# Performance work log

Measured on AMD Instinct MI355X. Metric: run time of the kernel, lower is better.

The kernel has to match this reference:

```python
import jax, jax.numpy as jnp
import numpy as np

B, LQ, LK, DQ, DKEY, DV = 8, 2048, 2048, 1024, 1024, 1024
MASK_NEG = -1e6  # d2l masked_softmax fill value


def setup_inputs() -> dict:
    key = jax.random.key(0)
    kq, kk, kv, kl, kw = jax.random.split(key, 5)
    queries = jax.random.normal(kq, (B, LQ, DQ), dtype=jnp.float32)
    keys = jax.random.normal(kk, (B, LK, DKEY), dtype=jnp.float32)
    values = jax.random.normal(kv, (B, LK, DV), dtype=jnp.float32)
    valid_lens = jax.random.randint(kl, (B,), 1, LK + 1)
    W_q = jax.random.normal(kw, (DQ, DKEY), dtype=jnp.float32) / np.sqrt(DQ)
    return {"queries": queries, "keys": keys, "values": values,
            "valid_lens": valid_lens, "W_q": W_q}


def reference(queries, keys, values, valid_lens, W_q):
    # Q projection: LazyLinear(key_dim, bias=False)
    q = jnp.einsum("bqd,dk->bqk", queries, W_q)          # [B, LQ, DKEY]
    d = q.shape[-1]
    scores = jnp.einsum("bqk,bsk->bqs", q, keys) / jnp.sqrt(jnp.asarray(d, q.dtype))
    # masked_softmax: positions >= valid_len set to -1e6 before softmax
    mask = jnp.arange(scores.shape[-1])[None, None, :] < valid_lens[:, None, None]
    scores = jnp.where(mask, scores, MASK_NEG)
    attn = jax.nn.softmax(scores, axis=-1)               # [B, LQ, LK]
    # dropout p=0.0 (eval) -> identity
    return jnp.einsum("bqs,bsv->bqv", attn, values)      # [B, LQ, DV]
```

## Files before the change

### kernel.cpp

```cpp
#include <hip/hip_runtime.h>
#include <cstdint>
#include <cstddef>

#define B_   8
#define LQ_  2048
#define LK_  2048

typedef __attribute__((ext_vector_type(8))) __bf16 bf16x8;
typedef __attribute__((ext_vector_type(4))) float f32x4;
typedef __attribute__((ext_vector_type(8))) unsigned short ushortx8;

__device__ __forceinline__ unsigned short f2bf(float f) {
  unsigned u = __builtin_bit_cast(unsigned, f);
  u = u + 0x7fffu + ((u >> 16) & 1u);
  return (unsigned short)(u >> 16);
}
__device__ __forceinline__ float bf2f(unsigned short h) {
  unsigned u = ((unsigned)h) << 16;
  return __builtin_bit_cast(float, u);
}

__device__ __forceinline__ void gld_lds16(const void* g, void* l) {
  __builtin_amdgcn_global_load_lds((__attribute__((address_space(1))) void*)(void*)g,
                                   (__attribute__((address_space(3))) void*)l, 16, 0, 0);
}

__global__ __launch_bounds__(256) void cast3_bf16_kernel(
    const float* __restrict__ q, unsigned short* __restrict__ qo,
    const float* __restrict__ k, unsigned short* __restrict__ ko,
    const float* __restrict__ w, unsigned short* __restrict__ wo,
    const int* __restrict__ vlp) {
  int bb = (int)blockIdx.x;
  const float* in;
  unsigned short* out;
  if (bb < 8192) {
    in = q; out = qo;
  } else if (bb < 16384) {
    bb -= 8192;
    in = k; out = ko;
    int batch = bb >> 10;
    int row = (bb & 1023) * 2;
    int vl = vlp[batch];
    if (row >= ((vl + 255) & ~255)) return;
  } else {
    bb -= 16384;
    in = w; out = wo;
  }
  size_t i = ((size_t)bb * 256 + threadIdx.x) * 8;
  float4 a = *(const float4*)(in + i);
  float4 b = *(const float4*)(in + i + 4);
  ushortx8 o;
  o[0] = f2bf(a.x); o[1] = f2bf(a.y); o[2] = f2bf(a.z); o[3] = f2bf(a.w);
  o[4] = f2bf(b.x); o[5] = f2bf(b.y); o[6] = f2bf(b.z); o[7] = f2bf(b.w);
  *(ushortx8*)(out + i) = o;
}

__global__ __launch_bounds__(256) void transpose_cast_kernel(
    const float* __restrict__ in, unsigned short* __restrict__ out,
    int R, int C, long in_bstride, long out_bstride, const int* __restrict__ vlp) {
  __shared__ float t[32][33];
  int r0 = blockIdx.y * 32;
  if (vlp) {
    int kEnd = (vlp[blockIdx.z] + 63) & ~63;
    if (r0 >= kEnd) return;
  }
  const float* inb = in + (size_t)blockIdx.z * in_bstride;
  unsigned short* outb = out + (size_t)blockIdx.z * out_bstride;
  int c0 = blockIdx.x * 32;
  int tx = threadIdx.x, ty = threadIdx.y;
#pragma unroll
  for (int k = 0; k < 4; ++k) {
    int r = ty + k * 8;
    t[r][tx] = inb[(size_t)(r0 + r) * C + c0 + tx];
  }
  __syncthreads();
#pragma unroll
  for (int k = 0; k < 4; ++k) {
    int c = ty + k * 8;
    outb[(size_t)(c0 + c) * R + r0 + tx] = f2bf(t[tx][c]);
  }
}

template <int OUTM, int SKIPN, int SKIPM, int CLAMPK>
__global__ __launch_bounds__(512, 2) void gemm256_kernel(
    const unsigned short* __restrict__ A, const unsigned short* __restrict__ B,
    void* __restrict__ Cp, int M, int N, int K,
    long a_bstride, long b_bstride, long c_bstride, float scale,
    const int* __restrict__ vlp) {
  __shared__ unsigned short lds[4][2][128 * 64];

  const int tid = threadIdx.x;
  const int wid = tid >> 6;
  const int lane = tid & 63;
  const int lane15 = lane & 15;
  const int lhalf = lane >> 4;

  const int nt = (int)((blockIdx.x + 2 * blockIdx.z) & (gridDim.x - 1));
  const int m0 = blockIdx.y * 256;
  const int n0 = nt * 256;

  int vl = K;
  if constexpr (SKIPN || SKIPM || CLAMPK) vl = vlp[blockIdx.z];
  if constexpr (SKIPN) {
    if (n0 >= vl) return;
  }
  if constexpr (SKIPM) {
    if (m0 >= vl) return;
  }
  int kEnd = K;
  if constexpr (CLAMPK) {
    int ke = (vl + 63) & ~63;
    kEnd = ke < K ? ke : K;
  }
  const int nKt = kEnd >> 5;

  const unsigned short* Ab = A + (size_t)blockIdx.z * a_bstride;
  const unsigned short* Bb = B + (size_t)blockIdx.z * b_bstride;

  int srowA[2], srowB[2], scol[2], sdst[2];
#pragma unroll
  for (int j = 0; j < 2; ++j) {
    int blk = (wid * 2 + j) * 64 + lane;
    int p = blk >> 3, q = blk & 7;
    int c = q ^ (p & 7);
    int r = 2 * p + (c >> 2);
    scol[j] = (c & 3) * 8;
    srowA[j] = m0 + r;
    srowB[j] = n0 + r;
    sdst[j] = blk * 8;
  }

  const int om = (wid >> 2) * 128;
  const int on = (wid & 3) * 64;
  const int swz8 = ((((lane15 & 1) << 2) + lhalf) ^ ((lane15 >> 1) & 7)) << 3;
  const int aBase = ((om >> 1) + (lane15 >> 1)) * 64 + swz8;
  const int bBase = ((on >> 1) + (lane15 >> 1)) * 64 + swz8;

  f32x4 acc[8][4];
#pragma unroll
  for (int f = 0; f < 8; ++f)
#pragma unroll
    for (int g = 0; g < 4; ++g) acc[f][g] = (f32x4){0.f, 0.f, 0.f, 0.f};

#pragma unroll
  for (int j = 0; j < 2; ++j)
    gld_lds16(Ab + (size_t)srowA[j] * K + scol[j], &lds[0][0][sdst[j]]);
#pragma unroll
  for (int j = 0; j < 2; ++j)
    gld_lds16(Bb + (size_t)srowB[j] * K + scol[j], &lds[0][1][sdst[j]]);
#pragma unroll
  for (int j = 0; j < 2; ++j)
    gld_lds16(Ab + (size_t)srowA[j] * K + (32 + scol[j]), &lds[1][0][sdst[j]]);
#pragma unroll
  for (int j = 0; j < 2; ++j)
    gld_lds16(Bb + (size_t)srowB[j] * K + (32 + scol[j]), &lds[1][1][sdst[j]]);
  if (nKt > 2) {
#pragma unroll
    for (int j = 0; j < 2; ++j)
      gld_lds16(Ab + (size_t)srowA[j] * K + (64 + scol[j]), &lds[2][0][sdst[j]]);
#pragma unroll
    for (int j = 0; j < 2; ++j)
      gld_lds16(Bb + (size_t)srowB[j] * K + (64 + scol[j]), &lds[2][1][sdst[j]]);
    asm volatile("s_waitcnt vmcnt(8)" ::: "memory");
  } else {
    asm volatile("s_waitcnt vmcnt(4)" ::: "memory");
  }
  __builtin_amdgcn_s_barrier();

  for (int t = 0; t < nKt; ++t) {
    const unsigned short* lA = &lds[t & 3][0][0];
    const unsigned short* lB = &lds[t & 3][1][0];
    const bool st = (t + 3) < nKt;
    const int nb = (t + 3) & 3;
    const int kc = (t + 3) * 32;

    bf16x8 a0[4], b0[4];
#pragma unroll
    for (int f = 0; f < 4; ++f) a0[f] = *(const bf16x8*)&lA[aBase + f * 512];
#pragma unroll
    for (int g = 0; g < 4; ++g) b0[g] = *(const bf16x8*)&lB[bBase + g * 512];
    if (st) {
#pragma unroll
      for (int j = 0; j < 2; ++j)
        gld_lds16(Ab + (size_t)srowA[j] * K + (kc + scol[j]), &lds[nb][0][sdst[j]]);
    }
    __builtin_amdgcn_s_barrier();
    asm volatile("s_waitcnt lgkmcnt(0)" ::: "memory");
    __builtin_amdgcn_sched_barrier(0);
    __builtin_amdgcn_s_setprio(1);
#pragma unroll
    for (int f = 0; f < 4; ++f)
#pragma unroll
      for (int g = 0; g < 4; ++g)
        acc[f][g] = __builtin_amdgcn_mfma_f32_16x16x32_bf16(a0[f], b0[g], acc[f][g], 0, 0, 0);
    __builtin_amdgcn_s_setprio(0);
    __builtin_amdgcn_s_barrier();

    bf16x8 a1[4];
#pragma unroll
    for (int f = 0; f < 4; ++f) a1[f] = *(const bf16x8*)&lA[aBase + (f + 4) * 512];
    if (st) {
#pragma unroll
      for (int j = 0; j < 2; ++j)
        gld_lds16(Bb + (size_t)srowB[j] * K + (kc + scol[j]), &lds[nb][1][sdst[j]]);
    }
    __builtin_amdgcn_s_barrier();
    asm volatile("s_waitcnt lgkmcnt(0)" ::: "memory");
    __builtin_amdgcn_sched_barrier(0);
    __builtin_amdgcn_s_setprio(1);
#pragma unroll
    for (int f = 0; f < 4; ++f)
#pragma unroll
      for (int g = 0; g < 4; ++g)
        acc[f + 4][g] = __builtin_amdgcn_mfma_f32_16x16x32_bf16(a1[f], b0[g], acc[f + 4][g], 0, 0, 0);
    __builtin_amdgcn_s_setprio(0);
    {
      int hi = nKt < t + 4 ? nKt : t + 4;
      int pend = hi - (t + 2);
      if (pend >= 2)
        asm volatile("s_waitcnt vmcnt(8)" ::: "memory");
      else if (pend == 1)
        asm volatile("s_waitcnt vmcnt(4)" ::: "memory");
      else
        asm volatile("s_waitcnt vmcnt(0)" ::: "memory");
    }
    __builtin_amdgcn_s_barrier();
  }

  const size_t boffC = (size_t)blockIdx.z * c_bstride;
#pragma unroll
  for (int f = 0; f < 8; ++f) {
    int row = m0 + om + f * 16 + lhalf * 4;
#pragma unroll
    for (int g = 0; g < 4; ++g) {
      int col = n0 + on + g * 16 + lane15;
#pragma unroll
      for (int r = 0; r < 4; ++r) {
        float v = acc[f][g][r];
        if constexpr (OUTM == 0) {
          ((unsigned short*)Cp + boffC)[(size_t)(row + r) * N + col] = f2bf(v);
        } else if constexpr (OUTM == 1) {
          ((unsigned short*)Cp + boffC)[(size_t)(row + r) * N + col] = f2bf(v * scale);
        } else {
          ((float*)Cp + boffC)[(size_t)(row + r) * N + col] = v;
        }
      }
    }
  }
}

__global__ __launch_bounds__(256) void softmax_kernel(unsigned short* __restrict__ scores,
                                                      const int* __restrict__ valid_lens) {
  const int row = blockIdx.x;
  const int b = row >> 11;
  const int vl = valid_lens[b];
  const int kEnd = (vl + 63) & ~63;
  unsigned short* rp = scores + (size_t)row * LK_;
  const int tid = threadIdx.x;
  const int wid = tid >> 6, lane = tid & 63;
  __shared__ float sred[4];

  const int cb = tid * 8;
  const bool act = cb < kEnd;
  ushortx8 h = {};
  if (act) h = *(const ushortx8*)(rp + cb);
  float x[8];
#pragma unroll
  for (int t = 0; t < 8; ++t) x[t] = bf2f(h[t]);

  float m = -3.4e38f;
#pragma unroll
  for (int t = 0; t < 8; ++t)
    if (cb + t < vl) m = fmaxf(m, x[t]);
#pragma unroll
  for (int off = 32; off >= 1; off >>= 1) m = fmaxf(m, __shfl_xor(m, off));
  if (lane == 0) sred[wid] = m;
  __syncthreads();
  m = fmaxf(fmaxf(sred[0], sred[1]), fmaxf(sred[2], sred[3]));
  __syncthreads();

  float e[8];
  float s = 0.f;
#pragma unroll
  for (int t = 0; t < 8; ++t) {
    e[t] = (cb + t < vl) ? __expf(x[t] - m) : 0.f;
    s += e[t];
  }
#pragma unroll
  for (int off = 32; off >= 1; off >>= 1) s += __shfl_xor(s, off);
  if (lane == 0) sred[wid] = s;
  __syncthreads();
  s = sred[0] + sred[1] + sred[2] + sred[3];
  float inv = 1.f / s;

  if (act) {
    ushortx8 o;
#pragma unroll
    for (int t = 0; t < 8; ++t) o[t] = f2bf(e[t] * inv);
    *(ushortx8*)(rp + cb) = o;
  }
}

extern "C" void kernel_launch(void* const* d_in, const int* in_sizes, int n_in,
                              void* d_out, int out_size, void* d_ws, size_t ws_size,
                              hipStream_t stream) {
  const float* queries = (const float*)d_in[0];
  const float* keys = (const float*)d_in[1];
  const float* values = (const float*)d_in[2];
  const int* valid_lens = (const int*)d_in[3];
  const float* W_q = (const float*)d_in[4];
  float* out = (float*)d_out;

  unsigned short* ws = (unsigned short*)d_ws;
  const size_t M1 = (size_t)1024 * 1024;
  unsigned short* q_bf = ws;
  unsigned short* scores = ws + 16 * M1;
  unsigned short* keysP = ws + 48 * M1;
  unsigned short* valsT = keysP;
  unsigned short* w_bf = ws + 64 * M1;
  unsigned short* keys_bf = ws + 65 * M1;

  cast3_bf16_kernel<<<dim3(16896), 256, 0, stream>>>(
      queries, q_bf, keys, keys_bf, W_q, w_bf, valid_lens);
  gemm256_kernel<0, 0, 1, 0><<<dim3(4, 8, 8), 512, 0, stream>>>(
      keys_bf, w_bf, keysP, 2048, 1024, 1024,
      (long)2048 * 1024, 0, (long)2048 * 1024, 1.f, valid_lens);
  gemm256_kernel<1, 1, 0, 0><<<dim3(8, 8, 8), 512, 0, stream>>>(
      q_bf, keysP, scores, 2048, 2048, 1024,
      (long)2048 * 1024, (long)2048 * 1024, (long)2048 * 2048, 0.03125f, valid_lens);
  transpose_cast_kernel<<<dim3(32, 64, 8), dim3(32, 8), 0, stream>>>(
      values, valsT, 2048, 1024, (long)2048 * 1024, (long)1024 * 2048, valid_lens);
  softmax_kernel<<<dim3(B_ * LQ_), 256, 0, stream>>>(scores, valid_lens);
  gemm256_kernel<2, 0, 0, 1><<<dim3(4, 8, 8), 512, 0, stream>>>(
      scores, valsT, out, 2048, 1024, 2048,
      (long)2048 * 2048, (long)1024 * 2048, (long)2048 * 1024, 1.f, valid_lens);
}
```

Before: 381.3 us.

## Double-buffer MFMA fragments in registers and cut barriers per K-step

Rewrites the GEMM main loop as a macro, unrolled by two, that ping-pongs two sets of A/B fragment registers. The next K-tile's fragments are read from LDS while the current tile's second MFMA half runs, instead of waiting at the top of each step. Barriers drop from three to one per K-step, and the vmcnt waits are tightened so only the next tile has to have landed. This is meant to hide LDS read latency and synchronisation stalls, at the cost of more registers and an implicit assumption that the K-tile count is even.

```diff
diff --git a/kernel.cpp b/kernel.cpp
--- a/kernel.cpp
+++ b/kernel.cpp
@@ -81,6 +81,70 @@
   }
 }
 
+#define KT_ITER(T, CA0, CB0, NA0, NB0)                                          \
+  {                                                                             \
+    const unsigned short* lA = &lds[(T) & 3][0][0];                             \
+    const unsigned short* lAn = &lds[((T) + 1) & 3][0][0];                      \
+    const unsigned short* lBn = &lds[((T) + 1) & 3][1][0];                      \
+    const bool st = (T) + 3 < nKt;                                              \
+    const int nb = ((T) + 3) & 3;                                               \
+    const int kc = ((T) + 3) * 32;                                              \
+    const bool rd = (T) + 1 < nKt;                                              \
+    bf16x8 a1[4];                                                               \
+    _Pragma("unroll")                                                           \
+    for (int f = 0; f < 4; ++f)                                                 \
+      a1[f] = *(const bf16x8*)&lA[aBase + (f + 4) * 512];                       \
+    if (st) {                                                                   \
+      _Pragma("unroll")                                                         \
+      for (int j = 0; j < 2; ++j)                                               \
+        gld_lds16(Ab + (size_t)srowA[j] * K + (kc + scol[j]),                   \
+                  &lds[nb][0][sdst[j]]);                                        \
+    }                                                                           \
+    __builtin_amdgcn_sched_barrier(0);                                          \
+    __builtin_amdgcn_s_setprio(1);                                              \
+    _Pragma("unroll")                                                           \
+    for (int f = 0; f < 4; ++f) {                                               \
+      _Pragma("unroll")                                                         \
+      for (int g = 0; g < 4; ++g)                                               \
+        acc[f][g] = __builtin_amdgcn_mfma_f32_16x16x32_bf16(CA0[f], CB0[g],     \
+                                                            acc[f][g], 0, 0, 0);\
+    }                                                                           \
+    __builtin_amdgcn_s_setprio(0);                                              \
+    asm volatile("s_waitcnt lgkmcnt(0)" ::: "memory");                          \
+    __builtin_amdgcn_sched_barrier(0);                                          \
+    if (rd) {                                                                   \
+      _Pragma("unroll")                                                         \
+      for (int f = 0; f < 4; ++f)                                               \
+        NA0[f] = *(const bf16x8*)&lAn[aBase + f * 512];                         \
+      _Pragma("unroll")                                                         \
+      for (int g = 0; g < 4; ++g)                                               \
+        NB0[g] = *(const bf16x8*)&lBn[bBase + g * 512];                         \
+    }                                                                           \
+    if (st) {                                                                   \
+      _Pragma("unroll")                                                         \
+      for (int j = 0; j < 2; ++j)                                               \
+        gld_lds16(Bb + (size_t)srowB[j] * K + (kc + scol[j]),                   \
+                  &lds[nb][1][sdst[j]]);                                        \
+    }                                                                           \
+    __builtin_amdgcn_sched_barrier(0);                                          \
+    __builtin_amdgcn_s_setprio(1);                                              \
+    _Pragma("unroll")                                                           \
+    for (int f = 0; f < 4; ++f) {                                               \
+      _Pragma("unroll")                                                         \
+      for (int g = 0; g < 4; ++g)                                               \
+        acc[f + 4][g] = __builtin_amdgcn_mfma_f32_16x16x32_bf16(                \
+            a1[f], CB0[g], acc[f + 4][g], 0, 0, 0);                             \
+    }                                                                           \
+    __builtin_amdgcn_s_setprio(0);                                              \
+    asm volatile("s_waitcnt lgkmcnt(0)" ::: "memory");                          \
+    if (st)                                                                     \
+      asm volatile("s_waitcnt vmcnt(4)" ::: "memory");                          \
+    else                                                                        \
+      asm volatile("s_waitcnt vmcnt(0)" ::: "memory");                          \
+    __builtin_amdgcn_sched_barrier(0);                                          \
+    __builtin_amdgcn_s_barrier();                                               \
+  }
+
 template <int OUTM, int SKIPN, int SKIPM, int CLAMPK>
 __global__ __launch_bounds__(512, 2) void gemm256_kernel(
     const unsigned short* __restrict__ A, const unsigned short* __restrict__ B,
@@ -161,70 +225,23 @@
 #pragma unroll
     for (int j = 0; j < 2; ++j)
       gld_lds16(Bb + (size_t)srowB[j] * K + (64 + scol[j]), &lds[2][1][sdst[j]]);
-    asm volatile("s_waitcnt vmcnt(8)" ::: "memory");
+    asm volatile("s_waitcnt vmcnt(4)" ::: "memory");
   } else {
-    asm volatile("s_waitcnt vmcnt(4)" ::: "memory");
+    asm volatile("s_waitcnt vmcnt(0)" ::: "memory");
   }
   __builtin_amdgcn_s_barrier();
 
-  for (int t = 0; t < nKt; ++t) {
-    const unsigned short* lA = &lds[t & 3][0][0];
-    const unsigned short* lB = &lds[t & 3][1][0];
-    const bool st = (t + 3) < nKt;
-    const int nb = (t + 3) & 3;
-    const int kc = (t + 3) * 32;
-
-    bf16x8 a0[4], b0[4];
-#pragma unroll
-    for (int f = 0; f < 4; ++f) a0[f] = *(const bf16x8*)&lA[aBase + f * 512];
-#pragma unroll
-    for (int g = 0; g < 4; ++g) b0[g] = *(const bf16x8*)&lB[bBase + g * 512];
-    if (st) {
-#pragma unroll
-      for (int j = 0; j < 2; ++j)
-        gld_lds16(Ab + (size_t)srowA[j] * K + (kc + scol[j]), &lds[nb][0][sdst[j]]);
-    }
-    __builtin_amdgcn_s_barrier();
-    asm volatile("s_waitcnt lgkmcnt(0)" ::: "memory");
-    __builtin_amdgcn_sched_barrier(0);
-    __builtin_amdgcn_s_setprio(1);
-#pragma unroll
-    for (int f = 0; f < 4; ++f)
-#pragma unroll
-      for (int g = 0; g < 4; ++g)
-        acc[f][g] = __builtin_amdgcn_mfma_f32_16x16x32_bf16(a0[f], b0[g], acc[f][g], 0, 0, 0);
-    __builtin_amdgcn_s_setprio(0);
-    __builtin_amdgcn_s_barrier();
-
-    bf16x8 a1[4];
-#pragma unroll
-    for (int f = 0; f < 4; ++f) a1[f] = *(const bf16x8*)&lA[aBase + (f + 4) * 512];
-    if (st) {
-#pragma unroll
-      for (int j = 0; j < 2; ++j)
-        gld_lds16(Bb + (size_t)srowB[j] * K + (kc + scol[j]), &lds[nb][1][sdst[j]]);
-    }
-    __builtin_amdgcn_s_barrier();
-    asm volatile("s_waitcnt lgkmcnt(0)" ::: "memory");
-    __builtin_amdgcn_sched_barrier(0);
-    __builtin_amdgcn_s_setprio(1);
-#pragma unroll
-    for (int f = 0; f < 4; ++f)
-#pragma unroll
-      for (int g = 0; g < 4; ++g)
-        acc[f + 4][g] = __builtin_amdgcn_mfma_f32_16x16x32_bf16(a1[f], b0[g], acc[f + 4][g], 0, 0, 0);
-    __builtin_amdgcn_s_setprio(0);
-    {
-      int hi = nKt < t + 4 ? nKt : t + 4;
-      int pend = hi - (t + 2);
-      if (pend >= 2)
-        asm volatile("s_waitcnt vmcnt(8)" ::: "memory");
-      else if (pend == 1)
-        asm volatile("s_waitcnt vmcnt(4)" ::: "memory");
-      else
-        asm volatile("s_waitcnt vmcnt(0)" ::: "memory");
-    }
-    __builtin_amdgcn_s_barrier();
+  bf16x8 a0X[4], b0X[4], a0Y[4], b0Y[4];
+#pragma unroll
+  for (int f = 0; f < 4; ++f) a0X[f] = *(const bf16x8*)&lds[0][0][aBase + f * 512];
+#pragma unroll
+  for (int g = 0; g < 4; ++g) b0X[g] = *(const bf16x8*)&lds[0][1][bBase + g * 512];
+  asm volatile("s_waitcnt lgkmcnt(0)" ::: "memory");
+  __builtin_amdgcn_sched_barrier(0);
+
+  for (int t = 0; t < nKt; t += 2) {
+    KT_ITER(t, a0X, b0X, a0Y, b0Y);
+    KT_ITER(t + 1, a0Y, b0Y, a0X, b0X);
   }
 
   const size_t boffC = (size_t)blockIdx.z * c_bstride;
```

Result: faster. 361.5 us (-5.2%).

## Shrink GEMM tiles to 128x128 with 4 waves and batch-interleaved 1D grid

Applied to the files above, without the earlier changes.

Replaces the 256x256 tile GEMM with 512 threads by a 128x128 tile GEMM with 256 threads and a flattened 1D grid where the batch index is the fastest-varying component. Finer tiles let the valid_len skipping (SKIPN/SKIPM) prune work at 128 granularity, and the key cast now also truncates at 128 rows. The intent is less wasted compute on masked regions and better load balance across CUs. The cost is lower arithmetic intensity per tile and more global/LDS traffic per FLOP. The in-loop pipeline is also simplified to a single MFMA phase per k-step, with one barrier removed.

```diff
diff --git a/kernel.cpp b/kernel.cpp
--- a/kernel.cpp
+++ b/kernel.cpp
@@ -41,7 +41,7 @@
     int batch = bb >> 10;
     int row = (bb & 1023) * 2;
     int vl = vlp[batch];
-    if (row >= ((vl + 255) & ~255)) return;
+    if (row >= ((vl + 127) & ~127)) return;
   } else {
     bb -= 16384;
     in = w; out = wo;
@@ -82,12 +82,12 @@
 }
 
 template <int OUTM, int SKIPN, int SKIPM, int CLAMPK>
-__global__ __launch_bounds__(512, 2) void gemm256_kernel(
+__global__ __launch_bounds__(256, 2) void gemm128_kernel(
     const unsigned short* __restrict__ A, const unsigned short* __restrict__ B,
     void* __restrict__ Cp, int M, int N, int K,
     long a_bstride, long b_bstride, long c_bstride, float scale,
-    const int* __restrict__ vlp) {
-  __shared__ unsigned short lds[4][2][128 * 64];
+    const int* __restrict__ vlp, int lognx) {
+  __shared__ unsigned short lds[4][2][64 * 64];
 
   const int tid = threadIdx.x;
   const int wid = tid >> 6;
@@ -95,12 +95,18 @@
   const int lane15 = lane & 15;
   const int lhalf = lane >> 4;
 
-  const int nt = (int)((blockIdx.x + 2 * blockIdx.z) & (gridDim.x - 1));
-  const int m0 = blockIdx.y * 256;
-  const int n0 = nt * 256;
+  const int idx = (int)blockIdx.x;
+  const int z = idx & 7;
+  const int rest = idx >> 3;
+  const int nxm = (1 << lognx) - 1;
+  const int xt = rest & nxm;
+  const int yt = rest >> lognx;
+  const int nt = (xt + 2 * z) & nxm;
+  const int m0 = yt * 128;
+  const int n0 = nt * 128;
 
   int vl = K;
-  if constexpr (SKIPN || SKIPM || CLAMPK) vl = vlp[blockIdx.z];
+  if constexpr (SKIPN || SKIPM || CLAMPK) vl = vlp[z];
   if constexpr (SKIPN) {
     if (n0 >= vl) return;
   }
@@ -114,8 +120,8 @@
   }
   const int nKt = kEnd >> 5;
 
-  const unsigned short* Ab = A + (size_t)blockIdx.z * a_bstride;
-  const unsigned short* Bb = B + (size_t)blockIdx.z * b_bstride;
+  const unsigned short* Ab = A + (size_t)z * a_bstride;
+  const unsigned short* Bb = B + (size_t)z * b_bstride;
 
   int srowA[2], srowB[2], scol[2], sdst[2];
 #pragma unroll
@@ -130,15 +136,15 @@
     sdst[j] = blk * 8;
   }
 
-  const int om = (wid >> 2) * 128;
-  const int on = (wid & 3) * 64;
+  const int om = (wid & 1) * 64;
+  const int on = (wid >> 1) * 64;
   const int swz8 = ((((lane15 & 1) << 2) + lhalf) ^ ((lane15 >> 1) & 7)) << 3;
   const int aBase = ((om >> 1) + (lane15 >> 1)) * 64 + swz8;
   const int bBase = ((on >> 1) + (lane15 >> 1)) * 64 + swz8;
 
-  f32x4 acc[8][4];
-#pragma unroll
-  for (int f = 0; f < 8; ++f)
+  f32x4 acc[4][4];
+#pragma unroll
+  for (int f = 0; f < 4; ++f)
 #pragma unroll
     for (int g = 0; g < 4; ++g) acc[f][g] = (f32x4){0.f, 0.f, 0.f, 0.f};
 
@@ -174,17 +180,19 @@
     const int nb = (t + 3) & 3;
     const int kc = (t + 3) * 32;
 
-    bf16x8 a0[4], b0[4];
-#pragma unroll
-    for (int f = 0; f < 4; ++f) a0[f] = *(const bf16x8*)&lA[aBase + f * 512];
-#pragma unroll
-    for (int g = 0; g < 4; ++g) b0[g] = *(const bf16x8*)&lB[bBase + g * 512];
+    bf16x8 a[4], b[4];
+#pragma unroll
+    for (int f = 0; f < 4; ++f) a[f] = *(const bf16x8*)&lA[aBase + f * 512];
+#pragma unroll
+    for (int g = 0; g < 4; ++g) b[g] = *(const bf16x8*)&lB[bBase + g * 512];
     if (st) {
 #pragma unroll
       for (int j = 0; j < 2; ++j)
         gld_lds16(Ab + (size_t)srowA[j] * K + (kc + scol[j]), &lds[nb][0][sdst[j]]);
+#pragma unroll
+      for (int j = 0; j < 2; ++j)
+        gld_lds16(Bb + (size_t)srowB[j] * K + (kc + scol[j]), &lds[nb][1][sdst[j]]);
     }
-    __builtin_amdgcn_s_barrier();
     asm volatile("s_waitcnt lgkmcnt(0)" ::: "memory");
     __builtin_amdgcn_sched_barrier(0);
     __builtin_amdgcn_s_setprio(1);
@@ -192,27 +200,7 @@
     for (int f = 0; f < 4; ++f)
 #pragma unroll
       for (int g = 0; g < 4; ++g)
-        acc[f][g] = __builtin_amdgcn_mfma_f32_16x16x32_bf16(a0[f], b0[g], acc[f][g], 0, 0, 0);
-    __builtin_amdgcn_s_setprio(0);
-    __builtin_amdgcn_s_barrier();
-
-    bf16x8 a1[4];
-#pragma unroll
-    for (int f = 0; f < 4; ++f) a1[f] = *(const bf16x8*)&lA[aBase + (f + 4) * 512];
-    if (st) {
-#pragma unroll
-      for (int j = 0; j < 2; ++j)
-        gld_lds16(Bb + (size_t)srowB[j] * K + (kc + scol[j]), &lds[nb][1][sdst[j]]);
-    }
-    __builtin_amdgcn_s_barrier();
-    asm volatile("s_waitcnt lgkmcnt(0)" ::: "memory");
-    __builtin_amdgcn_sched_barrier(0);
-    __builtin_amdgcn_s_setprio(1);
-#pragma unroll
-    for (int f = 0; f < 4; ++f)
-#pragma unroll
-      for (int g = 0; g < 4; ++g)
-        acc[f + 4][g] = __builtin_amdgcn_mfma_f32_16x16x32_bf16(a1[f], b0[g], acc[f + 4][g], 0, 0, 0);
+        acc[f][g] = __builtin_amdgcn_mfma_f32_16x16x32_bf16(a[f], b[g], acc[f][g], 0, 0, 0);
     __builtin_amdgcn_s_setprio(0);
     {
       int hi = nKt < t + 4 ? nKt : t + 4;
@@ -227,9 +215,9 @@
     __builtin_amdgcn_s_barrier();
   }
 
-  const size_t boffC = (size_t)blockIdx.z * c_bstride;
-#pragma unroll
-  for (int f = 0; f < 8; ++f) {
+  const size_t boffC = (size_t)z * c_bstride;
+#pragma unroll
+  for (int f = 0; f < 4; ++f) {
     int row = m0 + om + f * 16 + lhalf * 4;
 #pragma unroll
     for (int g = 0; g < 4; ++g) {
@@ -322,16 +310,16 @@
 
   cast3_bf16_kernel<<<dim3(16896), 256, 0, stream>>>(
       queries, q_bf, keys, keys_bf, W_q, w_bf, valid_lens);
-  gemm256_kernel<0, 0, 1, 0><<<dim3(4, 8, 8), 512, 0, stream>>>(
+  gemm128_kernel<0, 0, 1, 0><<<dim3(16 * 8 * 8), 256, 0, stream>>>(
       keys_bf, w_bf, keysP, 2048, 1024, 1024,
-      (long)2048 * 1024, 0, (long)2048 * 1024, 1.f, valid_lens);
-  gemm256_kernel<1, 1, 0, 0><<<dim3(8, 8, 8), 512, 0, stream>>>(
+      (long)2048 * 1024, 0, (long)2048 * 1024, 1.f, valid_lens, 3);
+  gemm128_kernel<1, 1, 0, 0><<<dim3(16 * 16 * 8), 256, 0, stream>>>(
       q_bf, keysP, scores, 2048, 2048, 1024,
-      (long)2048 * 1024, (long)2048 * 1024, (long)2048 * 2048, 0.03125f, valid_lens);
+      (long)2048 * 1024, (long)2048 * 1024, (long)2048 * 2048, 0.03125f, valid_lens, 4);
   transpose_cast_kernel<<<dim3(32, 64, 8), dim3(32, 8), 0, stream>>>(
       values, valsT, 2048, 1024, (long)2048 * 1024, (long)1024 * 2048, valid_lens);
   softmax_kernel<<<dim3(B_ * LQ_), 256, 0, stream>>>(scores, valid_lens);
-  gemm256_kernel<2, 0, 0, 1><<<dim3(4, 8, 8), 512, 0, stream>>>(
+  gemm128_kernel<2, 0, 0, 1><<<dim3(16 * 8 * 8), 256, 0, stream>>>(
       scores, valsT, out, 2048, 1024, 2048,
-      (long)2048 * 2048, (long)1024 * 2048, (long)2048 * 1024, 1.f, valid_lens);
-}
+      (long)2048 * 2048, (long)1024 * 2048, (long)2048 * 1024, 1.f, valid_lens, 3);
+}
```

After: 397.1 us. +4.1%, slower.
